# Performance work log

Hardware: AMD Instinct MI355X
Metric: run time of the kernel (lower is better)

The kernel has to match this reference:

```python
import jax, jax.numpy as jnp
import numpy as np

SAMPLE_RATE = 24000.0
SIGMA_MULT = 4.0
CHUNK = 512  # atoms processed per scan step (mirrors chunked Triton kernel)


def setup_inputs() -> dict:
    key = jax.random.key(0)
    ks = jax.random.split(key, 6)
    N = 4096
    num_samples = 72000  # 3 seconds at 24kHz
    duration = num_samples / SAMPLE_RATE
    amplitude = 0.1 * jax.random.normal(ks[0], (N,), dtype=jnp.float32)
    tau = jax.random.uniform(ks[1], (N,), dtype=jnp.float32) * duration
    omega = jax.random.uniform(ks[2], (N,), dtype=jnp.float32) * 8000.0
    sigma = 0.002 + jax.random.uniform(ks[3], (N,), dtype=jnp.float32) * 0.020
    phi = jax.random.uniform(ks[4], (N,), dtype=jnp.float32) * (2.0 * np.pi)
    gamma = 500.0 * jax.random.normal(ks[5], (N,), dtype=jnp.float32)
    return {"amplitude": amplitude, "tau": tau, "omega": omega,
            "sigma": sigma, "phi": phi, "gamma": gamma,
            "num_samples": num_samples}


def _render(amplitude, tau, omega, sigma, phi, gamma, num_samples):
    t = jnp.arange(num_samples, dtype=jnp.float32) / SAMPLE_RATE  # [T]
    two_pi = jnp.float32(2.0 * np.pi)

    def chunk_sum(acc, params):
        a, tu, om, sg, ph, gm = params  # each [CHUNK]
        tc = t[None, :] - tu[:, None]                    # [C,T]
        mask = jnp.abs(tc) <= SIGMA_MULT * sg[:, None]
        env = jnp.exp(-tc * tc / (2.0 * sg[:, None] ** 2 + 1e-8))
        phase = two_pi * (om[:, None] * tc + 0.5 * gm[:, None] * tc * tc) + ph[:, None]
        atoms = a[:, None] * env * jnp.cos(phase) * mask.astype(jnp.float32)
        return acc + atoms.sum(axis=0), None

    N = amplitude.shape[0]
    rs = lambda x: x.reshape(N // CHUNK, CHUNK)
    params = (rs(amplitude), rs(tau), rs(omega), rs(sigma), rs(phi), rs(gamma))
    out, _ = jax.lax.scan(chunk_sum, jnp.zeros((num_samples,), jnp.float32), params)
    return out


def reference(amplitude, tau, omega, sigma, phi, gamma, num_samples):
    return _render(amplitude, tau, omega, sigma, phi, gamma, num_samples)
```

## Files before the change

### kernel.cpp

```cpp
#include <hip/hip_runtime.h>
#include <math.h>


#define SR         24000.0f
#define TWO_PI     6.2831853071795864769f
#define LOG2E      1.4426950408889634f

#define TS     512
#define RBLOCK 128
#define SPT    4
#define SEGS   8
#define MAXA   512

__global__ void zero_kernel(float* __restrict__ out, int n_out,
                            int* __restrict__ counts, int n_cnt) {
    int i = blockIdx.x * blockDim.x + threadIdx.x;
    if (i < n_out) out[i] = 0.0f;
    if (i < n_cnt) counts[i] = 0;
}

__global__ void prep_kernel(const float* __restrict__ amp,
                            const float* __restrict__ tau,
                            const float* __restrict__ omega,
                            const float* __restrict__ sigma,
                            const float* __restrict__ phi,
                            const float* __restrict__ gamma,
                            float* __restrict__ params,
                            int* __restrict__ counts,
                            int* __restrict__ lists,
                            int N, int T, int ntiles) {
    int i = blockIdx.x * blockDim.x + threadIdx.x;
    if (i >= N) return;
    float a  = amp[i];
    float tu = tau[i];
    float om = omega[i];
    float sg = sigma[i];
    float ph = phi[i];
    float gm = gamma[i];

    float w   = 4.0f * sg;
    float k   = -LOG2E / (2.0f * sg * sg + 1e-8f);
    float phr = ph * (1.0f / TWO_PI);

    float* p = params + 8 * i;
    p[0] = a;  p[1] = tu; p[2] = om; p[3] = 0.5f * gm;
    p[4] = k;  p[5] = phr; p[6] = w; p[7] = 0.0f;

    int n_lo = (int)floorf((tu - w) * SR) - 1;
    int n_hi = (int)ceilf ((tu + w) * SR) + 1;
    if (n_lo < 0) n_lo = 0;
    if (n_hi > T - 1) n_hi = T - 1;
    if (n_lo > n_hi) return;

    int t0 = n_lo / TS, t1 = n_hi / TS;
    for (int tl = t0; tl <= t1; ++tl) {
        int pos = atomicAdd(&counts[tl], 1);
        if (pos < MAXA) lists[tl * MAXA + pos] = i;
    }
}

__global__ __launch_bounds__(RBLOCK) void render_kernel(
        const float* __restrict__ params,
        const int*   __restrict__ counts,
        const int*   __restrict__ lists,
        float*       __restrict__ out,
        int T) {
    __shared__ float4 s_par[RBLOCK][2];

    const int tile = blockIdx.x;
    const int seg  = blockIdx.y;
    const int tid  = threadIdx.x;
    const int s_base = tile * TS;
    const float t0 = (float)(s_base + tid) * (1.0f / SR);
    const float dt = (float)RBLOCK * (1.0f / SR);

    int cnt = counts[tile];
    if (cnt > MAXA) cnt = MAXA;
    const int per = (cnt + SEGS - 1) / SEGS;
    const int a0 = seg * per;
    const int a1 = min(cnt, a0 + per);

    const int* lst = lists + tile * MAXA;
    float acc[SPT] = {0.0f, 0.0f, 0.0f, 0.0f};

    for (int base = a0; base < a1; base += RBLOCK) {
        const int m = min(RBLOCK, a1 - base);
        __syncthreads();
        if (tid < m) {
            const int idx = lst[base + tid];
            const float4* p = (const float4*)(params + 8 * idx);
            s_par[tid][0] = p[0];
            s_par[tid][1] = p[1];
        }
        __syncthreads();

        for (int i = 0; i < m; ++i) {
            const float4 p0 = s_par[i][0];
            const float4 p1 = s_par[i][1];
            const float tc0 = t0 - p0.y;
            #pragma unroll
            for (int j = 0; j < SPT; ++j) {
                const float tc  = tc0 + (float)j * dt;
                const float tc2 = tc * tc;
                const float env = exp2f(p1.x * tc2);
                const float rev = fmaf(p0.z, tc, fmaf(p0.w, tc2, p1.y));
                const float r   = rev - floorf(rev);
                const float c   = __builtin_amdgcn_cosf(r);
                const float v   = p0.x * env * c;
                acc[j] += (fabsf(tc) <= p1.z) ? v : 0.0f;
            }
        }
    }

    #pragma unroll
    for (int j = 0; j < SPT; ++j) {
        const int t_idx = s_base + tid + j * RBLOCK;
        if (t_idx < T) atomicAdd(&out[t_idx], acc[j]);
    }
}

extern "C" void kernel_launch(void* const* d_in, const int* in_sizes, int n_in,
                              void* d_out, int out_size, void* d_ws, size_t ws_size,
                              hipStream_t stream) {
    const float* amp   = (const float*)d_in[0];
    const float* tau   = (const float*)d_in[1];
    const float* omega = (const float*)d_in[2];
    const float* sigma = (const float*)d_in[3];
    const float* phi   = (const float*)d_in[4];
    const float* gamma = (const float*)d_in[5];

    float* out = (float*)d_out;
    const int T = out_size;
    const int N = in_sizes[0];
    const int ntiles = (T + TS - 1) / TS;

    char* ws = (char*)d_ws;
    float* params = (float*)ws;
    int*   counts = (int*)(ws + (size_t)8 * N * sizeof(float));
    int*   lists  = (int*)(ws + (size_t)8 * N * sizeof(float) + (size_t)ntiles * sizeof(int));

    {
        int n = max(T, ntiles);
        zero_kernel<<<(n + 255) / 256, 256, 0, stream>>>(out, T, counts, ntiles);
    }
    prep_kernel<<<(N + 255) / 256, 256, 0, stream>>>(amp, tau, omega, sigma, phi, gamma,
                                                     params, counts, lists, N, T, ntiles);
    dim3 grid(ntiles, SEGS);
    render_kernel<<<grid, RBLOCK, 0, stream>>>(params, counts, lists, out, T);
}
```

Before: 96.56 us.

## Fuse zeroing with ballot-based tile binning and compute atom params in render

The separate zero kernel and the atomic-based prep kernel are replaced by one kernel. In it, each tile's wavefront scans all atoms and builds its own list with ballot and popcount, while the extra blocks zero the output with float4 stores. Atom parameters are now read and derived inside the render kernel, so the intermediate params buffer is gone. The per-sample window mask is removed from the inner loop. The aims are to save a launch and atomic contention and to shorten the hot loop. The cost is that atoms slightly outside their 4-sigma window now contribute small tail values within their tile, and every tile rescans all atoms.

```diff
diff --git a/kernel.cpp b/kernel.cpp
--- a/kernel.cpp
+++ b/kernel.cpp
@@ -12,55 +12,50 @@
 #define SEGS   8
 #define MAXA   512
 
-__global__ void zero_kernel(float* __restrict__ out, int n_out,
-                            int* __restrict__ counts, int n_cnt) {
-    int i = blockIdx.x * blockDim.x + threadIdx.x;
-    if (i < n_out) out[i] = 0.0f;
-    if (i < n_cnt) counts[i] = 0;
-}
+__global__ __launch_bounds__(64) void prep_kernel(
+        const float* __restrict__ tau,
+        const float* __restrict__ sigma,
+        int*   __restrict__ counts,
+        int*   __restrict__ lists,
+        float* __restrict__ out,
+        int N, int T, int ntiles) {
+    const int b    = blockIdx.x;
+    const int lane = threadIdx.x;
 
-__global__ void prep_kernel(const float* __restrict__ amp,
-                            const float* __restrict__ tau,
-                            const float* __restrict__ omega,
-                            const float* __restrict__ sigma,
-                            const float* __restrict__ phi,
-                            const float* __restrict__ gamma,
-                            float* __restrict__ params,
-                            int* __restrict__ counts,
-                            int* __restrict__ lists,
-                            int N, int T, int ntiles) {
-    int i = blockIdx.x * blockDim.x + threadIdx.x;
-    if (i >= N) return;
-    float a  = amp[i];
-    float tu = tau[i];
-    float om = omega[i];
-    float sg = sigma[i];
-    float ph = phi[i];
-    float gm = gamma[i];
-
-    float w   = 4.0f * sg;
-    float k   = -LOG2E / (2.0f * sg * sg + 1e-8f);
-    float phr = ph * (1.0f / TWO_PI);
-
-    float* p = params + 8 * i;
-    p[0] = a;  p[1] = tu; p[2] = om; p[3] = 0.5f * gm;
-    p[4] = k;  p[5] = phr; p[6] = w; p[7] = 0.0f;
-
-    int n_lo = (int)floorf((tu - w) * SR) - 1;
-    int n_hi = (int)ceilf ((tu + w) * SR) + 1;
-    if (n_lo < 0) n_lo = 0;
-    if (n_hi > T - 1) n_hi = T - 1;
-    if (n_lo > n_hi) return;
-
-    int t0 = n_lo / TS, t1 = n_hi / TS;
-    for (int tl = t0; tl <= t1; ++tl) {
-        int pos = atomicAdd(&counts[tl], 1);
-        if (pos < MAXA) lists[tl * MAXA + pos] = i;
+    if (b < ntiles) {
+        const float tstart = (float)(b * TS) * (1.0f / SR);
+        const float tend   = (float)(b * TS + TS - 1) * (1.0f / SR);
+        const float slack  = 2.0f / SR;
+        int cnt = 0;
+        for (int c = 0; c < N; c += 64) {
+            const int ai = c + lane;
+            bool hit = false;
+            if (ai < N) {
+                const float tu = tau[ai];
+                const float w  = 4.0f * sigma[ai] + slack;
+                hit = ((tu - w) <= tend) && ((tu + w) >= tstart);
+            }
+            const unsigned long long m = __ballot(hit);
+            if (hit) {
+                const int pos = cnt + (int)__popcll(m & ((1ull << lane) - 1ull));
+                if (pos < MAXA) lists[b * MAXA + pos] = ai;
+            }
+            cnt += (int)__popcll(m);
+        }
+        if (lane == 0) counts[b] = (cnt < MAXA) ? cnt : MAXA;
+    } else {
+        const int i4 = (b - ntiles) * 64 + lane;
+        if (i4 * 4 < T) ((float4*)out)[i4] = make_float4(0.f, 0.f, 0.f, 0.f);
     }
 }
 
 __global__ __launch_bounds__(RBLOCK) void render_kernel(
-        const float* __restrict__ params,
+        const float* __restrict__ amp,
+        const float* __restrict__ tau,
+        const float* __restrict__ omega,
+        const float* __restrict__ sigma,
+        const float* __restrict__ phi,
+        const float* __restrict__ gamma,
         const int*   __restrict__ counts,
         const int*   __restrict__ lists,
         float*       __restrict__ out,
@@ -75,7 +70,6 @@
     const float dt = (float)RBLOCK * (1.0f / SR);
 
     int cnt = counts[tile];
-    if (cnt > MAXA) cnt = MAXA;
     const int per = (cnt + SEGS - 1) / SEGS;
     const int a0 = seg * per;
     const int a1 = min(cnt, a0 + per);
@@ -88,9 +82,15 @@
         __syncthreads();
         if (tid < m) {
             const int idx = lst[base + tid];
-            const float4* p = (const float4*)(params + 8 * idx);
-            s_par[tid][0] = p[0];
-            s_par[tid][1] = p[1];
+            const float a  = amp[idx];
+            const float tu = tau[idx];
+            const float om = omega[idx];
+            const float sg = sigma[idx];
+            const float ph = phi[idx];
+            const float gm = gamma[idx];
+            const float k  = -LOG2E / (2.0f * sg * sg + 1e-8f);
+            s_par[tid][0] = make_float4(a, tu, om, 0.5f * gm);
+            s_par[tid][1] = make_float4(k, ph * (1.0f / TWO_PI), 0.0f, 0.0f);
         }
         __syncthreads();
 
@@ -106,8 +106,7 @@
                 const float rev = fmaf(p0.z, tc, fmaf(p0.w, tc2, p1.y));
                 const float r   = rev - floorf(rev);
                 const float c   = __builtin_amdgcn_cosf(r);
-                const float v   = p0.x * env * c;
-                acc[j] += (fabsf(tc) <= p1.z) ? v : 0.0f;
+                acc[j] = fmaf(p0.x * env, c, acc[j]);
             }
         }
     }
@@ -115,7 +114,7 @@
     #pragma unroll
     for (int j = 0; j < SPT; ++j) {
         const int t_idx = s_base + tid + j * RBLOCK;
-        if (t_idx < T) atomicAdd(&out[t_idx], acc[j]);
+        if (t_idx < T && a1 > a0) atomicAdd(&out[t_idx], acc[j]);
     }
 }
 
@@ -135,16 +134,13 @@
     const int ntiles = (T + TS - 1) / TS;
 
     char* ws = (char*)d_ws;
-    float* params = (float*)ws;
-    int*   counts = (int*)(ws + (size_t)8 * N * sizeof(float));
-    int*   lists  = (int*)(ws + (size_t)8 * N * sizeof(float) + (size_t)ntiles * sizeof(int));
+    int* counts = (int*)ws;
+    int* lists  = (int*)(ws + (size_t)ntiles * sizeof(int));
 
-    {
-        int n = max(T, ntiles);
-        zero_kernel<<<(n + 255) / 256, 256, 0, stream>>>(out, T, counts, ntiles);
-    }
-    prep_kernel<<<(N + 255) / 256, 256, 0, stream>>>(amp, tau, omega, sigma, phi, gamma,
-                                                     params, counts, lists, N, T, ntiles);
+    const int zblocks = (T / 4 + 63) / 64;
+    prep_kernel<<<ntiles + zblocks, 64, 0, stream>>>(tau, sigma, counts, lists,
+                                                     out, N, T, ntiles);
     dim3 grid(ntiles, SEGS);
-    render_kernel<<<grid, RBLOCK, 0, stream>>>(params, counts, lists, out, T);
+    render_kernel<<<grid, RBLOCK, 0, stream>>>(amp, tau, omega, sigma, phi, gamma,
+                                               counts, lists, out, T);
 }
```

After: 95.34 us. Within noise of the previous version (-1.3%).
